# Performance work log

Hardware: AMD Instinct MI355X
Metric: run time of the kernel (lower is better)

The kernel has to match this reference:

```python
import jax, jax.numpy as jnp
import numpy as np

NUM_HEADS = 16
NHID = 64
D = NUM_HEADS * NHID  # 1024, also keys/query/values dim and out_dim
SL, BS = 2048, 32


def setup_inputs() -> dict:
    key = jax.random.key(0)
    ks = jax.random.split(key, 7)
    s = 1.0 / np.sqrt(D)
    return {
        "query": jax.random.normal(ks[0], (BS, D), jnp.float32),
        "keys": jax.random.normal(ks[1], (SL, BS, D), jnp.float32),
        "values": jax.random.normal(ks[2], (SL, BS, D), jnp.float32),
        "Wq": jax.random.normal(ks[3], (D, D), jnp.float32) * s,
        "Wk": jax.random.normal(ks[4], (D, D), jnp.float32) * s,
        "Wv": jax.random.normal(ks[5], (D, D), jnp.float32) * s,
        "Wo": jax.random.normal(ks[6], (D, D), jnp.float32) * s,
    }


def reference(query, keys, values, Wq, Wk, Wv, Wo):
    sl, bs, _ = keys.shape
    qp = query @ Wq.T                       # [bs, H*nhid]
    kp = keys @ Wk.T                        # [sl, bs, H*nhid]
    vp = values @ Wv.T                      # [sl, bs, H*nhid]
    # elementwise multiplicative score, reduced per head
    dot = (qp * kp).reshape(sl, bs, NUM_HEADS, NHID).sum(-1) / np.sqrt(NHID)
    # NOTE: original uses log_softmax (not softmax) over the sequence dim
    w = jax.nn.log_softmax(dot, axis=0)[..., None]        # [sl, bs, H, 1]
    attn = (w * vp.reshape(sl, bs, NUM_HEADS, NHID)).sum(0)  # [bs, H, nhid]
    return attn.reshape(bs, -1) @ Wo.T                     # [bs, D]
```

## Files before the change

### kernel.cpp

```cpp
#include <hip/hip_runtime.h>

#define SL  2048
#define BSZ 32
#define DIM 1024
#define NH  16
#define HD  64

typedef __attribute__((ext_vector_type(4))) float f32x4;
typedef __attribute__((ext_vector_type(8))) short s16x8;

static __device__ __forceinline__ short f2bf(float f) {
    union { float f; unsigned u; } v; v.f = f;
    unsigned r = (v.u + 0x7fffu + ((v.u >> 16) & 1u)) >> 16;
    return (short)r;
}

__global__ __launch_bounds__(256) void k_qu(const float* __restrict__ query,
                                            const float* __restrict__ Wq,
                                            const float* __restrict__ Wk,
                                            short* __restrict__ u) {
    int b = blockIdx.x & 31;
    int h = blockIdx.x >> 5;
    int t = threadIdx.x;
    __shared__ float red[256];
    __shared__ float sq[HD];
    {
        int i  = t >> 2;
        int kq = t & 3;
        const float* q = query + (size_t)b * DIM + kq * 256;
        const float* w = Wq + (size_t)(h * HD + i) * DIM + kq * 256;
        f32x4 acc = {0.f, 0.f, 0.f, 0.f};
#pragma unroll 4
        for (int k = 0; k < 256; k += 4)
            acc += *(const f32x4*)(q + k) * *(const f32x4*)(w + k);
        red[t] = acc[0] + acc[1] + acc[2] + acc[3];
    }
    __syncthreads();
    if (t < HD) sq[t] = (red[t*4] + red[t*4+1] + red[t*4+2] + red[t*4+3]) * 0.125f;
    __syncthreads();
    f32x4 acc = {0.f, 0.f, 0.f, 0.f};
    const float* wk = Wk + (size_t)(h * HD) * DIM;
#pragma unroll 8
    for (int i = 0; i < HD; ++i) {
        float s = sq[i];
        const float* row = wk + (size_t)i * DIM;
        acc[0] += s * row[t];
        acc[1] += s * row[t + 256];
        acc[2] += s * row[t + 512];
        acc[3] += s * row[t + 768];
    }
    short* ub = u + ((size_t)(b * NH + h)) * DIM;
    ub[t]       = f2bf(acc[0]);
    ub[t + 256] = f2bf(acc[1]);
    ub[t + 512] = f2bf(acc[2]);
    ub[t + 768] = f2bf(acc[3]);
}

__global__ __launch_bounds__(256, 4) void k_dot(const float* __restrict__ keys,
                                                const short* __restrict__ u,
                                                float* __restrict__ dot,
                                                float2* __restrict__ part) {
    int b  = blockIdx.x & 31;
    int st = blockIdx.x >> 5;
    int s0 = st * 64;
    __shared__ short ulds[NH][DIM + 8];
    {
        const uint4* src = (const uint4*)(u + (size_t)b * NH * DIM);
        for (int idx = threadIdx.x; idx < NH * DIM / 8; idx += 256) {
            int row = idx >> 7;
            int col = (idx & 127) * 8;
            *(uint4*)&ulds[row][col] = src[idx];
        }
    }
    __syncthreads();
    int lane = threadIdx.x & 63;
    int wave = threadIdx.x >> 6;
    int lrow = lane & 15;
    int kgrp = lane >> 4;
    f32x4 acc = {0.f, 0.f, 0.f, 0.f};
    const float* ka = keys + ((size_t)(s0 + wave * 16 + lrow) * BSZ + b) * DIM;
#pragma unroll 4
    for (int k0 = 0; k0 < DIM; k0 += 32) {
        int kj = k0 + kgrp * 8;
        s16x8 bf = *(const s16x8*)&ulds[lrow][kj];
        f32x4 a0 = *(const f32x4*)(ka + kj);
        f32x4 a1 = *(const f32x4*)(ka + kj + 4);
        s16x8 af;
        af[0]=f2bf(a0[0]); af[1]=f2bf(a0[1]); af[2]=f2bf(a0[2]); af[3]=f2bf(a0[3]);
        af[4]=f2bf(a1[0]); af[5]=f2bf(a1[1]); af[6]=f2bf(a1[2]); af[7]=f2bf(a1[3]);
        acc = __builtin_amdgcn_mfma_f32_16x16x32_bf16(af, bf, acc, 0, 0, 0);
    }
    size_t obase = ((size_t)b * SL + (s0 + wave * 16 + kgrp * 4)) * NH + lrow;
#pragma unroll
    for (int r = 0; r < 4; ++r)
        dot[obase + (size_t)r * NH] = acc[r];

    __shared__ float mred[4][16], lred[4][16];
    float m = fmaxf(fmaxf(acc[0], acc[1]), fmaxf(acc[2], acc[3]));
    m = fmaxf(m, __shfl_xor(m, 16));
    m = fmaxf(m, __shfl_xor(m, 32));
    if (lane < 16) mred[wave][lrow] = m;
    __syncthreads();
    float mb = fmaxf(fmaxf(mred[0][lrow], mred[1][lrow]),
                     fmaxf(mred[2][lrow], mred[3][lrow]));
    float l = __expf(acc[0]-mb) + __expf(acc[1]-mb) + __expf(acc[2]-mb) + __expf(acc[3]-mb);
    l += __shfl_xor(l, 16);
    l += __shfl_xor(l, 32);
    if (lane < 16) lred[wave][lrow] = l;
    __syncthreads();
    int t = threadIdx.x;
    if (t < 16) {
        float mbb = fmaxf(fmaxf(mred[0][t], mred[1][t]), fmaxf(mred[2][t], mred[3][t]));
        float lb  = lred[0][t] + lred[1][t] + lred[2][t] + lred[3][t];
        part[((size_t)b * 32 + st) * 16 + t] = make_float2(mbb, lb);
    }
}

__global__ __launch_bounds__(256, 4) void k_z(const float* __restrict__ values,
                                              const float* __restrict__ w,
                                              const float2* __restrict__ part,
                                              float* __restrict__ z) {
    int x  = blockIdx.x;
    int b  = x & 31;
    int jc = (x >> 5) & 15;
    int sh = x >> 9;
    int t  = threadIdx.x;
    int ssub = t >> 4;
    int jq = t & 15;
    int j = jc * 64 + jq * 4;
    int wv = __builtin_amdgcn_readfirstlane(t >> 6);
    int lane = t & 63;

    __shared__ float wlds[128 * 16];
    __shared__ float Tl[16];
    __shared__ float mred8[8][16], lred8[8][16];
    __shared__ f32x4 redW[4][16][16];
    __shared__ f32x4 redV[4][16];

    if (t < 128) {
        int h = t & 15, g = t >> 4;
        const float2* pb = part + (size_t)b * 32 * 16 + h;
        float2 p0 = pb[(g*4+0)*16], p1 = pb[(g*4+1)*16],
               p2 = pb[(g*4+2)*16], p3 = pb[(g*4+3)*16];
        float M = fmaxf(fmaxf(p0.x, p1.x), fmaxf(p2.x, p3.x));
        float L = p0.y*__expf(p0.x-M) + p1.y*__expf(p1.x-M)
                + p2.y*__expf(p2.x-M) + p3.y*__expf(p3.x-M);
        mred8[g][h] = M; lred8[g][h] = L;
    }
    __syncthreads();
    if (t < 16) {
        float M = mred8[0][t];
#pragma unroll
        for (int g = 1; g < 8; ++g) M = fmaxf(M, mred8[g][t]);
        float L = 0.f;
#pragma unroll
        for (int g = 0; g < 8; ++g) L += lred8[g][t] * __expf(mred8[g][t] - M);
        Tl[t] = M + __logf(L);
    }

    f32x4 acc[NH];
#pragma unroll
    for (int h = 0; h < NH; ++h) acc[h] = (f32x4){0.f,0.f,0.f,0.f};
    f32x4 accV = {0.f,0.f,0.f,0.f};

    const float* vbase = values + (size_t)b * DIM + j;
    const float* wbase = w + ((size_t)b * SL + sh * 1024) * NH;

    for (int ph = 0; ph < 8; ++ph) {
        __syncthreads();
        {
            const f32x4* src = (const f32x4*)(wbase + ph * 128 * NH);
            f32x4* dst = (f32x4*)wlds;
            dst[t]       = src[t];
            dst[t + 256] = src[t + 256];
        }
        __syncthreads();
        int sbase = sh * 1024 + ph * 128;
#pragma unroll 4
        for (int it = 0; it < 8; ++it) {
            int s_loc = it * 16 + ssub;
            f32x4 v = *(const f32x4*)(vbase + (size_t)(sbase + s_loc) * (BSZ * DIM));
            const float* wr = wlds + s_loc * 16;
#pragma unroll
            for (int h = 0; h < NH; ++h) {
                float wh = wr[h];
                acc[h] += v * wh;
            }
            accV += v;
        }
    }

#pragma unroll
    for (int h = 0; h < NH; ++h) {
#pragma unroll
        for (int e = 0; e < 4; ++e) {
            float x0 = acc[h][e];
            x0 += __shfl_xor(x0, 16);
            x0 += __shfl_xor(x0, 32);
            acc[h][e] = x0;
        }
    }
#pragma unroll
    for (int e = 0; e < 4; ++e) {
        float x0 = accV[e];
        x0 += __shfl_xor(x0, 16);
        x0 += __shfl_xor(x0, 32);
        accV[e] = x0;
    }
    if (lane < 16) {
#pragma unroll
        for (int h = 0; h < NH; ++h) redW[wv][h][lane] = acc[h];
        redV[wv][lane] = accV;
    }
    __syncthreads();
    int h2 = t >> 4, q = t & 15;
    f32x4 sumW = redW[0][h2][q] + redW[1][h2][q] + redW[2][h2][q] + redW[3][h2][q];
    f32x4 sumV = redV[0][q] + redV[1][q] + redV[2][q] + redV[3][q];
    float Th = Tl[h2];
    f32x4 zv = sumW - Th * sumV;
    float* zp = z + (size_t)sh * (BSZ * NH * DIM);
    *(f32x4*)(zp + ((size_t)(b * NH + h2)) * DIM + jc * 64 + q * 4) = zv;
}

template<bool DUAL>
__global__ __launch_bounds__(256) void k_gemm(const float* __restrict__ A,
                                              const float* __restrict__ A2,
                                              const float* __restrict__ W,
                                              float* __restrict__ O,
                                              int rmul, int hsel) {
    int oc = blockIdx.x & 15;
    int b  = blockIdx.x >> 4;
    int wv = __builtin_amdgcn_readfirstlane(threadIdx.x >> 6);
    int lane = threadIdx.x & 63;
    int o = oc * 64 + lane;
    int row = b * rmul + (hsel ? oc : 0);
    const float* arow  = A + (size_t)row * DIM + wv * 256;
    const float* a2row = DUAL ? (A2 + (size_t)row * DIM + wv * 256) : nullptr;
    const float* wrow  = W + (size_t)o * DIM + wv * 256;
    f32x4 acc = {0.f, 0.f, 0.f, 0.f};
#pragma unroll 4
    for (int k = 0; k < 256; k += 4) {
        f32x4 a = *(const f32x4*)(arow + k);
        if (DUAL) a += *(const f32x4*)(a2row + k);
        f32x4 w = *(const f32x4*)(wrow + k);
        acc += a * w;
    }
    __shared__ float red[4][64];
    red[wv][lane] = acc[0] + acc[1] + acc[2] + acc[3];
    __syncthreads();
    int t = threadIdx.x;
    if (t < 64)
        O[(size_t)b * DIM + oc * 64 + t] = red[0][t] + red[1][t] + red[2][t] + red[3][t];
}

extern "C" void kernel_launch(void* const* d_in, const int* in_sizes, int n_in,
                              void* d_out, int out_size, void* d_ws, size_t ws_size,
                              hipStream_t stream) {
    const float* query  = (const float*)d_in[0];
    const float* keys   = (const float*)d_in[1];
    const float* values = (const float*)d_in[2];
    const float* Wq = (const float*)d_in[3];
    const float* Wk = (const float*)d_in[4];
    const float* Wv = (const float*)d_in[5];
    const float* Wo = (const float*)d_in[6];
    float* out = (float*)d_out;

    char* ws = (char*)d_ws;
    short*  u    = (short*)(ws + 0);
    float*  dotb = (float*)(ws + (1 << 20));
    float*  z0   = (float*)(ws + (5 << 20));
    float*  z1   = (float*)(ws + (7 << 20));
    float*  attn = (float*)(ws + (9 << 20));
    float2* part = (float2*)(ws + (9 << 20) + (128 << 10));

    hipLaunchKernelGGL(k_qu,          dim3(512),  dim3(256), 0, stream, query, Wq, Wk, u);
    hipLaunchKernelGGL(k_dot,         dim3(1024), dim3(256), 0, stream, keys, u, dotb, part);
    hipLaunchKernelGGL(k_z,           dim3(1024), dim3(256), 0, stream, values, dotb, part, z0);
    hipLaunchKernelGGL(k_gemm<true>,  dim3(512),  dim3(256), 0, stream, z0, z1, Wv, attn, 16, 1);
    hipLaunchKernelGGL(k_gemm<false>, dim3(512),  dim3(256), 0, stream, attn, nullptr, Wo, out, 1, 0);
}
```

Measured before the change: 207.9 us.

## Restructure dot, value-reduction and Wv projection kernels with new work split

The dot kernel now processes 16 sequence rows per block (4096 blocks). Each block stages bf16-converted keys in LDS, and the four waves split the K dimension and reduce their MFMA partials through shared memory. The value-weighted reduction becomes k_zpart: 256 blocks of 512 threads, each streaming 256 sequence steps with float2 loads, writing 8 sequence-split partials plus value sums. The log-sum-exp finalisation and the partial combine move into the Wv GEMM kernel, which removes the separate normalisation from the z kernel. This trades more workspace traffic (8 partial z buffers) and low block count in k_zpart for better occupancy in the dot stage.

```diff
diff --git a/kernel.cpp b/kernel.cpp
--- a/kernel.cpp
+++ b/kernel.cpp
@@ -56,197 +56,199 @@
     ub[t + 768] = f2bf(acc[3]);
 }
 
-__global__ __launch_bounds__(256, 4) void k_dot(const float* __restrict__ keys,
-                                                const short* __restrict__ u,
-                                                float* __restrict__ dot,
-                                                float2* __restrict__ part) {
+__global__ __launch_bounds__(256) void k_dot2(const float* __restrict__ keys,
+                                              const short* __restrict__ u,
+                                              float* __restrict__ dot,
+                                              float2* __restrict__ part) {
     int b  = blockIdx.x & 31;
     int st = blockIdx.x >> 5;
-    int s0 = st * 64;
+    int s0 = st * 16;
     __shared__ short ulds[NH][DIM + 8];
+    __shared__ short klds[16][DIM + 8];
+    __shared__ f32x4 redc[4][64];
+    int t = threadIdx.x;
+    int w = t >> 6, l = t & 63;
+
     {
         const uint4* src = (const uint4*)(u + (size_t)b * NH * DIM);
-        for (int idx = threadIdx.x; idx < NH * DIM / 8; idx += 256) {
+        for (int idx = t; idx < NH * DIM / 8; idx += 256) {
             int row = idx >> 7;
             int col = (idx & 127) * 8;
             *(uint4*)&ulds[row][col] = src[idx];
         }
     }
-    __syncthreads();
-    int lane = threadIdx.x & 63;
-    int wave = threadIdx.x >> 6;
-    int lrow = lane & 15;
-    int kgrp = lane >> 4;
+#pragma unroll
+    for (int r = 0; r < 4; ++r) {
+        int srow = w * 4 + r;
+        const float* kr = keys + ((size_t)(s0 + srow) * BSZ + b) * DIM;
+#pragma unroll
+        for (int kq = 0; kq < 4; ++kq) {
+            f32x4 v = *(const f32x4*)(kr + kq * 256 + l * 4);
+            ushort4 o;
+            o.x = (unsigned short)f2bf(v[0]);
+            o.y = (unsigned short)f2bf(v[1]);
+            o.z = (unsigned short)f2bf(v[2]);
+            o.w = (unsigned short)f2bf(v[3]);
+            *(ushort4*)&klds[srow][kq * 256 + l * 4] = o;
+        }
+    }
+    __syncthreads();
+
+    int lrow = l & 15, kgrp = l >> 4;
     f32x4 acc = {0.f, 0.f, 0.f, 0.f};
-    const float* ka = keys + ((size_t)(s0 + wave * 16 + lrow) * BSZ + b) * DIM;
+#pragma unroll
+    for (int kk = 0; kk < 8; ++kk) {
+        int kj = w * 256 + kk * 32 + kgrp * 8;
+        s16x8 af = *(const s16x8*)&klds[lrow][kj];
+        s16x8 bf = *(const s16x8*)&ulds[lrow][kj];
+        acc = __builtin_amdgcn_mfma_f32_16x16x32_bf16(af, bf, acc, 0, 0, 0);
+    }
+    redc[w][l] = acc;
+    __syncthreads();
+    if (t < 64) {
+        f32x4 sum = redc[0][t] + redc[1][t] + redc[2][t] + redc[3][t];
+        int lr = t & 15, kg = t >> 4;
+        size_t obase = ((size_t)b * SL + (s0 + kg * 4)) * NH + lr;
+#pragma unroll
+        for (int r = 0; r < 4; ++r)
+            dot[obase + (size_t)r * NH] = sum[r];
+        float m = fmaxf(fmaxf(sum[0], sum[1]), fmaxf(sum[2], sum[3]));
+        m = fmaxf(m, __shfl_xor(m, 16));
+        m = fmaxf(m, __shfl_xor(m, 32));
+        float lsum = __expf(sum[0]-m) + __expf(sum[1]-m) + __expf(sum[2]-m) + __expf(sum[3]-m);
+        lsum += __shfl_xor(lsum, 16);
+        lsum += __shfl_xor(lsum, 32);
+        if (t < 16)
+            part[((size_t)b * 128 + st) * 16 + t] = make_float2(m, lsum);
+    }
+}
+
+__global__ __launch_bounds__(512) void k_zpart(const float* __restrict__ values,
+                                               const float* __restrict__ dotb,
+                                               float* __restrict__ zpart,
+                                               float* __restrict__ svpart) {
+    int b  = blockIdx.x & 31;
+    int sq = blockIdx.x >> 5;
+    int t  = threadIdx.x;
+    __shared__ f32x4 wlds4[1024];
+    {
+        const f32x4* src = (const f32x4*)(dotb + ((size_t)b * SL + sq * 256) * NH);
+        wlds4[t]       = src[t];
+        wlds4[t + 512] = src[t + 512];
+    }
+    __syncthreads();
+    const float* wlds = (const float*)wlds4;
+
+    float ax[NH], ay[NH];
+#pragma unroll
+    for (int h = 0; h < NH; ++h) { ax[h] = 0.f; ay[h] = 0.f; }
+    float svx = 0.f, svy = 0.f;
+
+    const float* vbase = values + ((size_t)(sq * 256) * BSZ + b) * DIM + t * 2;
+#pragma unroll 8
+    for (int s = 0; s < 256; ++s) {
+        float2 v = *(const float2*)(vbase + (size_t)s * (BSZ * DIM));
+        const float* wr = wlds + s * 16;
+#pragma unroll
+        for (int h = 0; h < NH; ++h) {
+            float wh = wr[h];
+            ax[h] += v.x * wh;
+            ay[h] += v.y * wh;
+        }
+        svx += v.x;
+        svy += v.y;
+    }
+    float* zp = zpart + (size_t)(sq * 32 + b) * NH * DIM + t * 2;
+#pragma unroll
+    for (int h = 0; h < NH; ++h) {
+        float2 o; o.x = ax[h]; o.y = ay[h];
+        *(float2*)(zp + (size_t)h * DIM) = o;
+    }
+    float2 sv; sv.x = svx; sv.y = svy;
+    *(float2*)(svpart + (size_t)(sq * 32 + b) * DIM + t * 2) = sv;
+}
+
+__global__ __launch_bounds__(256) void k_attn(const float* __restrict__ zpart,
+                                              const float* __restrict__ svpart,
+                                              const float2* __restrict__ part,
+                                              const float* __restrict__ Wv,
+                                              float* __restrict__ attn) {
+    int oc = blockIdx.x & 15;
+    int b  = blockIdx.x >> 4;
+    int t  = threadIdx.x;
+    int wv = t >> 6, l = t & 63;
+    __shared__ float mred[16][16], lred[16][16];
+    __shared__ float Tl[16];
+    __shared__ float arow[DIM];
+    __shared__ float red[4][64];
+    {
+        int h = t & 15, g = t >> 4;
+        const float2* pb = part + (size_t)b * 128 * 16 + h;
+        float M = -1e30f;
+        float2 ps[8];
+#pragma unroll
+        for (int i = 0; i < 8; ++i) ps[i] = pb[(size_t)(g * 8 + i) * 16];
+#pragma unroll
+        for (int i = 0; i < 8; ++i) M = fmaxf(M, ps[i].x);
+        float L = 0.f;
+#pragma unroll
+        for (int i = 0; i < 8; ++i) L += ps[i].y * __expf(ps[i].x - M);
+        mred[g][h] = M; lred[g][h] = L;
+    }
+    __syncthreads();
+    if (t < 16) {
+        float M = mred[0][t];
+#pragma unroll
+        for (int g = 1; g < 16; ++g) M = fmaxf(M, mred[g][t]);
+        float L = 0.f;
+#pragma unroll
+        for (int g = 0; g < 16; ++g) L += lred[g][t] * __expf(mred[g][t] - M);
+        Tl[t] = M + __logf(L);
+    }
+    __syncthreads();
+    {
+        int k = wv * 256 + l * 4;
+        f32x4 a = {0.f,0.f,0.f,0.f}, sv = {0.f,0.f,0.f,0.f};
+#pragma unroll
+        for (int p = 0; p < 8; ++p) {
+            a  += *(const f32x4*)(zpart + ((size_t)((p * 32 + b) * NH + oc)) * DIM + k);
+            sv += *(const f32x4*)(svpart + (size_t)(p * 32 + b) * DIM + k);
+        }
+        a -= Tl[oc] * sv;
+        *(f32x4*)&arow[k] = a;
+    }
+    __syncthreads();
+    const float* wr = Wv + (size_t)(oc * 64 + l) * DIM + wv * 256;
+    const float* ar = arow + wv * 256;
+    f32x4 acc = {0.f,0.f,0.f,0.f};
 #pragma unroll 4
-    for (int k0 = 0; k0 < DIM; k0 += 32) {
-        int kj = k0 + kgrp * 8;
-        s16x8 bf = *(const s16x8*)&ulds[lrow][kj];
-        f32x4 a0 = *(const f32x4*)(ka + kj);
-        f32x4 a1 = *(const f32x4*)(ka + kj + 4);
-        s16x8 af;
-        af[0]=f2bf(a0[0]); af[1]=f2bf(a0[1]); af[2]=f2bf(a0[2]); af[3]=f2bf(a0[3]);
-        af[4]=f2bf(a1[0]); af[5]=f2bf(a1[1]); af[6]=f2bf(a1[2]); af[7]=f2bf(a1[3]);
-        acc = __builtin_amdgcn_mfma_f32_16x16x32_bf16(af, bf, acc, 0, 0, 0);
-    }
-    size_t obase = ((size_t)b * SL + (s0 + wave * 16 + kgrp * 4)) * NH + lrow;
-#pragma unroll
-    for (int r = 0; r < 4; ++r)
-        dot[obase + (size_t)r * NH] = acc[r];
-
-    __shared__ float mred[4][16], lred[4][16];
-    float m = fmaxf(fmaxf(acc[0], acc[1]), fmaxf(acc[2], acc[3]));
-    m = fmaxf(m, __shfl_xor(m, 16));
-    m = fmaxf(m, __shfl_xor(m, 32));
-    if (lane < 16) mred[wave][lrow] = m;
-    __syncthreads();
-    float mb = fmaxf(fmaxf(mred[0][lrow], mred[1][lrow]),
-                     fmaxf(mred[2][lrow], mred[3][lrow]));
-    float l = __expf(acc[0]-mb) + __expf(acc[1]-mb) + __expf(acc[2]-mb) + __expf(acc[3]-mb);
-    l += __shfl_xor(l, 16);
-    l += __shfl_xor(l, 32);
-    if (lane < 16) lred[wave][lrow] = l;
-    __syncthreads();
-    int t = threadIdx.x;
-    if (t < 16) {
-        float mbb = fmaxf(fmaxf(mred[0][t], mred[1][t]), fmaxf(mred[2][t], mred[3][t]));
-        float lb  = lred[0][t] + lred[1][t] + lred[2][t] + lred[3][t];
-        part[((size_t)b * 32 + st) * 16 + t] = make_float2(mbb, lb);
-    }
-}
-
-__global__ __launch_bounds__(256, 4) void k_z(const float* __restrict__ values,
-                                              const float* __restrict__ w,
-                                              const float2* __restrict__ part,
-                                              float* __restrict__ z) {
-    int x  = blockIdx.x;
-    int b  = x & 31;
-    int jc = (x >> 5) & 15;
-    int sh = x >> 9;
-    int t  = threadIdx.x;
-    int ssub = t >> 4;
-    int jq = t & 15;
-    int j = jc * 64 + jq * 4;
-    int wv = __builtin_amdgcn_readfirstlane(t >> 6);
-    int lane = t & 63;
-
-    __shared__ float wlds[128 * 16];
-    __shared__ float Tl[16];
-    __shared__ float mred8[8][16], lred8[8][16];
-    __shared__ f32x4 redW[4][16][16];
-    __shared__ f32x4 redV[4][16];
-
-    if (t < 128) {
-        int h = t & 15, g = t >> 4;
-        const float2* pb = part + (size_t)b * 32 * 16 + h;
-        float2 p0 = pb[(g*4+0)*16], p1 = pb[(g*4+1)*16],
-               p2 = pb[(g*4+2)*16], p3 = pb[(g*4+3)*16];
-        float M = fmaxf(fmaxf(p0.x, p1.x), fmaxf(p2.x, p3.x));
-        float L = p0.y*__expf(p0.x-M) + p1.y*__expf(p1.x-M)
-                + p2.y*__expf(p2.x-M) + p3.y*__expf(p3.x-M);
-        mred8[g][h] = M; lred8[g][h] = L;
-    }
-    __syncthreads();
-    if (t < 16) {
-        float M = mred8[0][t];
-#pragma unroll
-        for (int g = 1; g < 8; ++g) M = fmaxf(M, mred8[g][t]);
-        float L = 0.f;
-#pragma unroll
-        for (int g = 0; g < 8; ++g) L += lred8[g][t] * __expf(mred8[g][t] - M);
-        Tl[t] = M + __logf(L);
-    }
-
-    f32x4 acc[NH];
-#pragma unroll
-    for (int h = 0; h < NH; ++h) acc[h] = (f32x4){0.f,0.f,0.f,0.f};
-    f32x4 accV = {0.f,0.f,0.f,0.f};
-
-    const float* vbase = values + (size_t)b * DIM + j;
-    const float* wbase = w + ((size_t)b * SL + sh * 1024) * NH;
-
-    for (int ph = 0; ph < 8; ++ph) {
-        __syncthreads();
-        {
-            const f32x4* src = (const f32x4*)(wbase + ph * 128 * NH);
-            f32x4* dst = (f32x4*)wlds;
-            dst[t]       = src[t];
-            dst[t + 256] = src[t + 256];
-        }
-        __syncthreads();
-        int sbase = sh * 1024 + ph * 128;
-#pragma unroll 4
-        for (int it = 0; it < 8; ++it) {
-            int s_loc = it * 16 + ssub;
-            f32x4 v = *(const f32x4*)(vbase + (size_t)(sbase + s_loc) * (BSZ * DIM));
-            const float* wr = wlds + s_loc * 16;
-#pragma unroll
-            for (int h = 0; h < NH; ++h) {
-                float wh = wr[h];
-                acc[h] += v * wh;
-            }
-            accV += v;
-        }
-    }
-
-#pragma unroll
-    for (int h = 0; h < NH; ++h) {
-#pragma unroll
-        for (int e = 0; e < 4; ++e) {
-            float x0 = acc[h][e];
-            x0 += __shfl_xor(x0, 16);
-            x0 += __shfl_xor(x0, 32);
-            acc[h][e] = x0;
-        }
-    }
-#pragma unroll
-    for (int e = 0; e < 4; ++e) {
-        float x0 = accV[e];
-        x0 += __shfl_xor(x0, 16);
-        x0 += __shfl_xor(x0, 32);
-        accV[e] = x0;
-    }
-    if (lane < 16) {
-#pragma unroll
-        for (int h = 0; h < NH; ++h) redW[wv][h][lane] = acc[h];
-        redV[wv][lane] = accV;
-    }
-    __syncthreads();
-    int h2 = t >> 4, q = t & 15;
-    f32x4 sumW = redW[0][h2][q] + redW[1][h2][q] + redW[2][h2][q] + redW[3][h2][q];
-    f32x4 sumV = redV[0][q] + redV[1][q] + redV[2][q] + redV[3][q];
-    float Th = Tl[h2];
-    f32x4 zv = sumW - Th * sumV;
-    float* zp = z + (size_t)sh * (BSZ * NH * DIM);
-    *(f32x4*)(zp + ((size_t)(b * NH + h2)) * DIM + jc * 64 + q * 4) = zv;
-}
-
-template<bool DUAL>
-__global__ __launch_bounds__(256) void k_gemm(const float* __restrict__ A,
-                                              const float* __restrict__ A2,
-                                              const float* __restrict__ W,
-                                              float* __restrict__ O,
-                                              int rmul, int hsel) {
+    for (int kk = 0; kk < 256; kk += 4)
+        acc += *(const f32x4*)(ar + kk) * *(const f32x4*)(wr + kk);
+    red[wv][l] = acc[0] + acc[1] + acc[2] + acc[3];
+    __syncthreads();
+    if (t < 64)
+        attn[(size_t)b * DIM + oc * 64 + t] = red[0][t] + red[1][t] + red[2][t] + red[3][t];
+}
+
+__global__ __launch_bounds__(256) void k_out(const float* __restrict__ A,
+                                             const float* __restrict__ W,
+                                             float* __restrict__ O) {
     int oc = blockIdx.x & 15;
     int b  = blockIdx.x >> 4;
     int wv = __builtin_amdgcn_readfirstlane(threadIdx.x >> 6);
-    int lane = threadIdx.x & 63;
-    int o = oc * 64 + lane;
-    int row = b * rmul + (hsel ? oc : 0);
-    const float* arow  = A + (size_t)row * DIM + wv * 256;
-    const float* a2row = DUAL ? (A2 + (size_t)row * DIM + wv * 256) : nullptr;
-    const float* wrow  = W + (size_t)o * DIM + wv * 256;
+    int l  = threadIdx.x & 63;
+    int o  = oc * 64 + l;
+    const float* arow = A + (size_t)b * DIM + wv * 256;
+    const float* wrow = W + (size_t)o * DIM + wv * 256;
     f32x4 acc = {0.f, 0.f, 0.f, 0.f};
 #pragma unroll 4
     for (int k = 0; k < 256; k += 4) {
         f32x4 a = *(const f32x4*)(arow + k);
-        if (DUAL) a += *(const f32x4*)(a2row + k);
         f32x4 w = *(const f32x4*)(wrow + k);
         acc += a * w;
     }
     __shared__ float red[4][64];
-    red[wv][lane] = acc[0] + acc[1] + acc[2] + acc[3];
+    red[wv][l] = acc[0] + acc[1] + acc[2] + acc[3];
     __syncthreads();
     int t = threadIdx.x;
     if (t < 64)
@@ -266,16 +268,16 @@
     float* out = (float*)d_out;
 
     char* ws = (char*)d_ws;
-    short*  u    = (short*)(ws + 0);
-    float*  dotb = (float*)(ws + (1 << 20));
-    float*  z0   = (float*)(ws + (5 << 20));
-    float*  z1   = (float*)(ws + (7 << 20));
-    float*  attn = (float*)(ws + (9 << 20));
-    float2* part = (float2*)(ws + (9 << 20) + (128 << 10));
-
-    hipLaunchKernelGGL(k_qu,          dim3(512),  dim3(256), 0, stream, query, Wq, Wk, u);
-    hipLaunchKernelGGL(k_dot,         dim3(1024), dim3(256), 0, stream, keys, u, dotb, part);
-    hipLaunchKernelGGL(k_z,           dim3(1024), dim3(256), 0, stream, values, dotb, part, z0);
-    hipLaunchKernelGGL(k_gemm<true>,  dim3(512),  dim3(256), 0, stream, z0, z1, Wv, attn, 16, 1);
-    hipLaunchKernelGGL(k_gemm<false>, dim3(512),  dim3(256), 0, stream, attn, nullptr, Wo, out, 1, 0);
-}
+    short*  u      = (short*)(ws + 0);
+    float*  dotb   = (float*)(ws + (1 << 20));
+    float2* part   = (float2*)(ws + (5 << 20));
+    float*  zpart  = (float*)(ws + (5 << 20) + (512 << 10));
+    float*  svpart = (float*)(ws + (21 << 20) + (512 << 10));
+    float*  attn   = (float*)(ws + (22 << 20) + (512 << 10));
+
+    hipLaunchKernelGGL(k_qu,    dim3(512),  dim3(256), 0, stream, query, Wq, Wk, u);
+    hipLaunchKernelGGL(k_dot2,  dim3(4096), dim3(256), 0, stream, keys, u, dotb, part);
+    hipLaunchKernelGGL(k_zpart, dim3(256),  dim3(512), 0, stream, values, dotb, zpart, svpart);
+    hipLaunchKernelGGL(k_attn,  dim3(512),  dim3(256), 0, stream, zpart, svpart, part, Wv, attn);
+    hipLaunchKernelGGL(k_out,   dim3(512),  dim3(256), 0, stream, attn, Wo, out);
+}
```

New measurement: 212.3 us. 2.1% more time.

## Fuse five kernels into one cooperative persistent kernel with grid syncs

Applied to the files above, without the earlier changes.

Merges the five phase kernels into a single cooperative launch that separates phases with grid.sync(), keeping a multi-kernel fallback if the cooperative launch fails. Shared memory is unioned across phases. The u tile in LDS now uses an XOR swizzle in place of row padding to avoid bank conflicts. This removes per-launch gaps and tail drain between kernels. In exchange, the LDS union raises the per-block footprint, so occupancy is limited to the largest phase, and grid-wide barriers carry their own cost.

```diff
diff --git a/kernel.cpp b/kernel.cpp
--- a/kernel.cpp
+++ b/kernel.cpp
@@ -1,4 +1,7 @@
 #include <hip/hip_runtime.h>
+#include <hip/hip_cooperative_groups.h>
+
+namespace cg = cooperative_groups;
 
 #define SL  2048
 #define BSZ 32
@@ -15,15 +18,25 @@
     return (short)r;
 }
 
-__global__ __launch_bounds__(256) void k_qu(const float* __restrict__ query,
-                                            const float* __restrict__ Wq,
-                                            const float* __restrict__ Wk,
-                                            short* __restrict__ u) {
-    int b = blockIdx.x & 31;
-    int h = blockIdx.x >> 5;
-    int t = threadIdx.x;
-    __shared__ float red[256];
-    __shared__ float sq[HD];
+union SharedU {
+    struct { float red[256]; float sq[HD]; } p1;
+    union {
+        short ulds[NH * 1024];
+        struct { float mred[4][16]; float lred[4][16]; } r;
+    } p2;
+    struct { float wlds[128 * 16]; float Tl[16];
+             float mred8[8][16]; float lred8[8][16];
+             f32x4 redW[4][16][16]; f32x4 redV[4][16]; } p3;
+    struct { float red[4][64]; } p45;
+};
+
+static __device__ __forceinline__ void phase_u(int blk, int t, SharedU* sh,
+                                               const float* __restrict__ query,
+                                               const float* __restrict__ Wq,
+                                               const float* __restrict__ Wk,
+                                               short* __restrict__ u) {
+    int b = blk & 31;
+    int h = blk >> 5;
     {
         int i  = t >> 2;
         int kq = t & 3;
@@ -33,16 +46,18 @@
 #pragma unroll 4
         for (int k = 0; k < 256; k += 4)
             acc += *(const f32x4*)(q + k) * *(const f32x4*)(w + k);
-        red[t] = acc[0] + acc[1] + acc[2] + acc[3];
-    }
-    __syncthreads();
-    if (t < HD) sq[t] = (red[t*4] + red[t*4+1] + red[t*4+2] + red[t*4+3]) * 0.125f;
+        sh->p1.red[t] = acc[0] + acc[1] + acc[2] + acc[3];
+    }
+    __syncthreads();
+    if (t < HD)
+        sh->p1.sq[t] = (sh->p1.red[t*4] + sh->p1.red[t*4+1] +
+                        sh->p1.red[t*4+2] + sh->p1.red[t*4+3]) * 0.125f;
     __syncthreads();
     f32x4 acc = {0.f, 0.f, 0.f, 0.f};
     const float* wk = Wk + (size_t)(h * HD) * DIM;
 #pragma unroll 8
     for (int i = 0; i < HD; ++i) {
-        float s = sq[i];
+        float s = sh->p1.sq[i];
         const float* row = wk + (size_t)i * DIM;
         acc[0] += s * row[t];
         acc[1] += s * row[t + 256];
@@ -56,33 +71,35 @@
     ub[t + 768] = f2bf(acc[3]);
 }
 
-__global__ __launch_bounds__(256, 4) void k_dot(const float* __restrict__ keys,
-                                                const short* __restrict__ u,
-                                                float* __restrict__ dot,
-                                                float2* __restrict__ part) {
-    int b  = blockIdx.x & 31;
-    int st = blockIdx.x >> 5;
+static __device__ __forceinline__ void phase_dot(int blk, int t, SharedU* sh,
+                                                 const float* __restrict__ keys,
+                                                 const short* __restrict__ u,
+                                                 float* __restrict__ dotb,
+                                                 float2* __restrict__ part) {
+    int b  = blk & 31;
+    int st = blk >> 5;
     int s0 = st * 64;
-    __shared__ short ulds[NH][DIM + 8];
+    short* ulds = sh->p2.ulds;
     {
         const uint4* src = (const uint4*)(u + (size_t)b * NH * DIM);
-        for (int idx = threadIdx.x; idx < NH * DIM / 8; idx += 256) {
+        for (int idx = t; idx < NH * DIM / 8; idx += 256) {
             int row = idx >> 7;
-            int col = (idx & 127) * 8;
-            *(uint4*)&ulds[row][col] = src[idx];
+            int c   = idx & 127;
+            *(uint4*)&ulds[row * 1024 + ((c ^ (row & 7)) << 3)] = src[idx];
         }
     }
     __syncthreads();
-    int lane = threadIdx.x & 63;
-    int wave = threadIdx.x >> 6;
+    int lane = t & 63;
+    int wave = t >> 6;
     int lrow = lane & 15;
     int kgrp = lane >> 4;
+    int swz  = (lrow & 7) << 3;
     f32x4 acc = {0.f, 0.f, 0.f, 0.f};
     const float* ka = keys + ((size_t)(s0 + wave * 16 + lrow) * BSZ + b) * DIM;
 #pragma unroll 4
     for (int k0 = 0; k0 < DIM; k0 += 32) {
         int kj = k0 + kgrp * 8;
-        s16x8 bf = *(const s16x8*)&ulds[lrow][kj];
+        s16x8 bf = *(const s16x8*)&ulds[lrow * 1024 + (kj ^ swz)];
         f32x4 a0 = *(const f32x4*)(ka + kj);
         f32x4 a1 = *(const f32x4*)(ka + kj + 4);
         s16x8 af;
@@ -93,69 +110,63 @@
     size_t obase = ((size_t)b * SL + (s0 + wave * 16 + kgrp * 4)) * NH + lrow;
 #pragma unroll
     for (int r = 0; r < 4; ++r)
-        dot[obase + (size_t)r * NH] = acc[r];
-
-    __shared__ float mred[4][16], lred[4][16];
+        dotb[obase + (size_t)r * NH] = acc[r];
+
+    __syncthreads();
     float m = fmaxf(fmaxf(acc[0], acc[1]), fmaxf(acc[2], acc[3]));
     m = fmaxf(m, __shfl_xor(m, 16));
     m = fmaxf(m, __shfl_xor(m, 32));
-    if (lane < 16) mred[wave][lrow] = m;
-    __syncthreads();
-    float mb = fmaxf(fmaxf(mred[0][lrow], mred[1][lrow]),
-                     fmaxf(mred[2][lrow], mred[3][lrow]));
-    float l = __expf(acc[0]-mb) + __expf(acc[1]-mb) + __expf(acc[2]-mb) + __expf(acc[3]-mb);
-    l += __shfl_xor(l, 16);
-    l += __shfl_xor(l, 32);
-    if (lane < 16) lred[wave][lrow] = l;
-    __syncthreads();
-    int t = threadIdx.x;
+    if (lane < 16) sh->p2.r.mred[wave][lrow] = m;
+    __syncthreads();
+    float mb = fmaxf(fmaxf(sh->p2.r.mred[0][lrow], sh->p2.r.mred[1][lrow]),
+                     fmaxf(sh->p2.r.mred[2][lrow], sh->p2.r.mred[3][lrow]));
+    float lsum = __expf(acc[0]-mb) + __expf(acc[1]-mb) + __expf(acc[2]-mb) + __expf(acc[3]-mb);
+    lsum += __shfl_xor(lsum, 16);
+    lsum += __shfl_xor(lsum, 32);
+    if (lane < 16) sh->p2.r.lred[wave][lrow] = lsum;
+    __syncthreads();
     if (t < 16) {
-        float mbb = fmaxf(fmaxf(mred[0][t], mred[1][t]), fmaxf(mred[2][t], mred[3][t]));
-        float lb  = lred[0][t] + lred[1][t] + lred[2][t] + lred[3][t];
+        float mbb = fmaxf(fmaxf(sh->p2.r.mred[0][t], sh->p2.r.mred[1][t]),
+                          fmaxf(sh->p2.r.mred[2][t], sh->p2.r.mred[3][t]));
+        float lb  = sh->p2.r.lred[0][t] + sh->p2.r.lred[1][t]
+                  + sh->p2.r.lred[2][t] + sh->p2.r.lred[3][t];
         part[((size_t)b * 32 + st) * 16 + t] = make_float2(mbb, lb);
     }
 }
 
-__global__ __launch_bounds__(256, 4) void k_z(const float* __restrict__ values,
-                                              const float* __restrict__ w,
-                                              const float2* __restrict__ part,
-                                              float* __restrict__ z) {
-    int x  = blockIdx.x;
-    int b  = x & 31;
-    int jc = (x >> 5) & 15;
-    int sh = x >> 9;
-    int t  = threadIdx.x;
+static __device__ __forceinline__ void phase_z(int blk, int t, SharedU* sh,
+                                               const float* __restrict__ values,
+                                               const float* __restrict__ dotb,
+                                               const float2* __restrict__ part,
+                                               float* __restrict__ z) {
+    int b   = blk & 31;
+    int jc  = (blk >> 5) & 15;
+    int shf = blk >> 9;
     int ssub = t >> 4;
     int jq = t & 15;
     int j = jc * 64 + jq * 4;
     int wv = __builtin_amdgcn_readfirstlane(t >> 6);
     int lane = t & 63;
 
-    __shared__ float wlds[128 * 16];
-    __shared__ float Tl[16];
-    __shared__ float mred8[8][16], lred8[8][16];
-    __shared__ f32x4 redW[4][16][16];
-    __shared__ f32x4 redV[4][16];
-
     if (t < 128) {
         int h = t & 15, g = t >> 4;
         const float2* pb = part + (size_t)b * 32 * 16 + h;
         float2 p0 = pb[(g*4+0)*16], p1 = pb[(g*4+1)*16],
-               p2 = pb[(g*4+2)*16], p3 = pb[(g*4+3)*16];
-        float M = fmaxf(fmaxf(p0.x, p1.x), fmaxf(p2.x, p3.x));
+               p2 = pb[(g*4+2)*16], p3v = pb[(g*4+3)*16];
+        float M = fmaxf(fmaxf(p0.x, p1.x), fmaxf(p2.x, p3v.x));
         float L = p0.y*__expf(p0.x-M) + p1.y*__expf(p1.x-M)
-                + p2.y*__expf(p2.x-M) + p3.y*__expf(p3.x-M);
-        mred8[g][h] = M; lred8[g][h] = L;
+                + p2.y*__expf(p2.x-M) + p3v.y*__expf(p3v.x-M);
+        sh->p3.mred8[g][h] = M; sh->p3.lred8[g][h] = L;
     }
     __syncthreads();
     if (t < 16) {
-        float M = mred8[0][t];
-#pragma unroll
-        for (int g = 1; g < 8; ++g) M = fmaxf(M, mred8[g][t]);
+        float M = sh->p3.mred8[0][t];
+#pragma unroll
+        for (int g = 1; g < 8; ++g) M = fmaxf(M, sh->p3.mred8[g][t]);
         float L = 0.f;
 #pragma unroll
-        for (int g = 0; g < 8; ++g) L += lred8[g][t] * __expf(mred8[g][t] - M);
-        Tl[t] = M + __logf(L);
+        for (int g = 0; g < 8; ++g) L += sh->p3.lred8[g][t] * __expf(sh->p3.mred8[g][t] - M);
+        sh->p3.Tl[t] = M + __logf(L);
     }
 
     f32x4 acc[NH];
@@ -164,23 +175,23 @@
     f32x4 accV = {0.f,0.f,0.f,0.f};
 
     const float* vbase = values + (size_t)b * DIM + j;
-    const float* wbase = w + ((size_t)b * SL + sh * 1024) * NH;
+    const float* wbase = dotb + ((size_t)b * SL + shf * 1024) * NH;
 
     for (int ph = 0; ph < 8; ++ph) {
         __syncthreads();
         {
             const f32x4* src = (const f32x4*)(wbase + ph * 128 * NH);
-            f32x4* dst = (f32x4*)wlds;
+            f32x4* dst = (f32x4*)sh->p3.wlds;
             dst[t]       = src[t];
             dst[t + 256] = src[t + 256];
         }
         __syncthreads();
-        int sbase = sh * 1024 + ph * 128;
+        int sbase = shf * 1024 + ph * 128;
 #pragma unroll 4
         for (int it = 0; it < 8; ++it) {
             int s_loc = it * 16 + ssub;
             f32x4 v = *(const f32x4*)(vbase + (size_t)(sbase + s_loc) * (BSZ * DIM));
-            const float* wr = wlds + s_loc * 16;
+            const float* wr = sh->p3.wlds + s_loc * 16;
 #pragma unroll
             for (int h = 0; h < NH; ++h) {
                 float wh = wr[h];
@@ -209,48 +220,118 @@
     }
     if (lane < 16) {
 #pragma unroll
-        for (int h = 0; h < NH; ++h) redW[wv][h][lane] = acc[h];
-        redV[wv][lane] = accV;
+        for (int h = 0; h < NH; ++h) sh->p3.redW[wv][h][lane] = acc[h];
+        sh->p3.redV[wv][lane] = accV;
     }
     __syncthreads();
     int h2 = t >> 4, q = t & 15;
-    f32x4 sumW = redW[0][h2][q] + redW[1][h2][q] + redW[2][h2][q] + redW[3][h2][q];
-    f32x4 sumV = redV[0][q] + redV[1][q] + redV[2][q] + redV[3][q];
-    float Th = Tl[h2];
+    f32x4 sumW = sh->p3.redW[0][h2][q] + sh->p3.redW[1][h2][q]
+               + sh->p3.redW[2][h2][q] + sh->p3.redW[3][h2][q];
+    f32x4 sumV = sh->p3.redV[0][q] + sh->p3.redV[1][q]
+               + sh->p3.redV[2][q] + sh->p3.redV[3][q];
+    float Th = sh->p3.Tl[h2];
     f32x4 zv = sumW - Th * sumV;
-    float* zp = z + (size_t)sh * (BSZ * NH * DIM);
+    float* zp = z + (size_t)shf * (BSZ * NH * DIM);
     *(f32x4*)(zp + ((size_t)(b * NH + h2)) * DIM + jc * 64 + q * 4) = zv;
 }
 
-template<bool DUAL>
-__global__ __launch_bounds__(256) void k_gemm(const float* __restrict__ A,
-                                              const float* __restrict__ A2,
-                                              const float* __restrict__ W,
-                                              float* __restrict__ O,
-                                              int rmul, int hsel) {
-    int oc = blockIdx.x & 15;
-    int b  = blockIdx.x >> 4;
-    int wv = __builtin_amdgcn_readfirstlane(threadIdx.x >> 6);
-    int lane = threadIdx.x & 63;
+static __device__ __forceinline__ void phase_attn(int blk, int t, SharedU* sh,
+                                                  const float* __restrict__ z,
+                                                  const float* __restrict__ Wv,
+                                                  float* __restrict__ attn) {
+    int oc = blk & 15;
+    int b  = blk >> 4;
+    int wv = __builtin_amdgcn_readfirstlane(t >> 6);
+    int lane = t & 63;
     int o = oc * 64 + lane;
-    int row = b * rmul + (hsel ? oc : 0);
-    const float* arow  = A + (size_t)row * DIM + wv * 256;
-    const float* a2row = DUAL ? (A2 + (size_t)row * DIM + wv * 256) : nullptr;
-    const float* wrow  = W + (size_t)o * DIM + wv * 256;
+    int row = b * 16 + oc;
+    const float* arow  = z + (size_t)row * DIM + wv * 256;
+    const float* a2row = z + (size_t)(BSZ * NH * DIM) + (size_t)row * DIM + wv * 256;
+    const float* wrow  = Wv + (size_t)o * DIM + wv * 256;
     f32x4 acc = {0.f, 0.f, 0.f, 0.f};
 #pragma unroll 4
     for (int k = 0; k < 256; k += 4) {
-        f32x4 a = *(const f32x4*)(arow + k);
-        if (DUAL) a += *(const f32x4*)(a2row + k);
-        f32x4 w = *(const f32x4*)(wrow + k);
-        acc += a * w;
-    }
-    __shared__ float red[4][64];
-    red[wv][lane] = acc[0] + acc[1] + acc[2] + acc[3];
-    __syncthreads();
+        f32x4 a = *(const f32x4*)(arow + k) + *(const f32x4*)(a2row + k);
+        acc += a * *(const f32x4*)(wrow + k);
+    }
+    sh->p45.red[wv][lane] = acc[0] + acc[1] + acc[2] + acc[3];
+    __syncthreads();
+    if (t < 64)
+        attn[(size_t)b * DIM + oc * 64 + t] =
+            sh->p45.red[0][t] + sh->p45.red[1][t] + sh->p45.red[2][t] + sh->p45.red[3][t];
+}
+
+static __device__ __forceinline__ void phase_out(int blk, int t, SharedU* sh,
+                                                 const float* __restrict__ attn,
+                                                 const float* __restrict__ Wo,
+                                                 float* __restrict__ out) {
+    int oc = blk & 15;
+    int b  = blk >> 4;
+    int wv = __builtin_amdgcn_readfirstlane(t >> 6);
+    int lane = t & 63;
+    int o = oc * 64 + lane;
+    const float* arow = attn + (size_t)b * DIM + wv * 256;
+    const float* wrow = Wo + (size_t)o * DIM + wv * 256;
+    f32x4 acc = {0.f, 0.f, 0.f, 0.f};
+#pragma unroll 4
+    for (int k = 0; k < 256; k += 4)
+        acc += *(const f32x4*)(arow + k) * *(const f32x4*)(wrow + k);
+    sh->p45.red[wv][lane] = acc[0] + acc[1] + acc[2] + acc[3];
+    __syncthreads();
+    if (t < 64)
+        out[(size_t)b * DIM + oc * 64 + t] =
+            sh->p45.red[0][t] + sh->p45.red[1][t] + sh->p45.red[2][t] + sh->p45.red[3][t];
+}
+
+__global__ __launch_bounds__(256, 4) void k_mega(
+    const float* __restrict__ query, const float* __restrict__ keys,
+    const float* __restrict__ values, const float* __restrict__ Wq,
+    const float* __restrict__ Wk, const float* __restrict__ Wv,
+    const float* __restrict__ Wo, short* __restrict__ u,
+    float* __restrict__ dotb, float2* __restrict__ part,
+    float* __restrict__ z, float* __restrict__ attn,
+    float* __restrict__ out)
+{
+    cg::grid_group grid = cg::this_grid();
+    __shared__ SharedU sh;
+    int blk = blockIdx.x;
     int t = threadIdx.x;
-    if (t < 64)
-        O[(size_t)b * DIM + oc * 64 + t] = red[0][t] + red[1][t] + red[2][t] + red[3][t];
+
+    if (blk < 512) phase_u(blk, t, &sh, query, Wq, Wk, u);
+    grid.sync();
+    phase_dot(blk, t, &sh, keys, u, dotb, part);
+    grid.sync();
+    phase_z(blk, t, &sh, values, dotb, part, z);
+    grid.sync();
+    if (blk < 512) phase_attn(blk, t, &sh, z, Wv, attn);
+    grid.sync();
+    if (blk < 512) phase_out(blk, t, &sh, attn, Wo, out);
+}
+
+__global__ __launch_bounds__(256, 4) void k_p1(const float* query, const float* Wq,
+                                               const float* Wk, short* u) {
+    __shared__ SharedU sh;
+    phase_u(blockIdx.x, threadIdx.x, &sh, query, Wq, Wk, u);
+}
+__global__ __launch_bounds__(256, 4) void k_p2(const float* keys, const short* u,
+                                               float* dotb, float2* part) {
+    __shared__ SharedU sh;
+    phase_dot(blockIdx.x, threadIdx.x, &sh, keys, u, dotb, part);
+}
+__global__ __launch_bounds__(256, 4) void k_p3(const float* values, const float* dotb,
+                                               const float2* part, float* z) {
+    __shared__ SharedU sh;
+    phase_z(blockIdx.x, threadIdx.x, &sh, values, dotb, part, z);
+}
+__global__ __launch_bounds__(256, 4) void k_p4(const float* z, const float* Wv,
+                                               float* attn) {
+    __shared__ SharedU sh;
+    phase_attn(blockIdx.x, threadIdx.x, &sh, z, Wv, attn);
+}
+__global__ __launch_bounds__(256, 4) void k_p5(const float* attn, const float* Wo,
+                                               float* out) {
+    __shared__ SharedU sh;
+    phase_out(blockIdx.x, threadIdx.x, &sh, attn, Wo, out);
 }
 
 extern "C" void kernel_launch(void* const* d_in, const int* in_sizes, int n_in,
@@ -263,19 +344,27 @@
     const float* Wk = (const float*)d_in[4];
     const float* Wv = (const float*)d_in[5];
     const float* Wo = (const float*)d_in[6];
-    float* out = (float*)d_out;
+    float* outp = (float*)d_out;
 
     char* ws = (char*)d_ws;
     short*  u    = (short*)(ws + 0);
     float*  dotb = (float*)(ws + (1 << 20));
-    float*  z0   = (float*)(ws + (5 << 20));
-    float*  z1   = (float*)(ws + (7 << 20));
-    float*  attn = (float*)(ws + (9 << 20));
-    float2* part = (float2*)(ws + (9 << 20) + (128 << 10));
-
-    hipLaunchKernelGGL(k_qu,          dim3(512),  dim3(256), 0, stream, query, Wq, Wk, u);
-    hipLaunchKernelGGL(k_dot,         dim3(1024), dim3(256), 0, stream, keys, u, dotb, part);
-    hipLaunchKernelGGL(k_z,           dim3(1024), dim3(256), 0, stream, values, dotb, part, z0);
-    hipLaunchKernelGGL(k_gemm<true>,  dim3(512),  dim3(256), 0, stream, z0, z1, Wv, attn, 16, 1);
-    hipLaunchKernelGGL(k_gemm<false>, dim3(512),  dim3(256), 0, stream, attn, nullptr, Wo, out, 1, 0);
-}
+    float2* part = (float2*)(ws + (5 << 20));
+    float*  z    = (float*)(ws + (5 << 20) + (512 << 10));
+    float*  attn = (float*)(ws + (9 << 20) + (512 << 10));
+
+    void* args[13] = {
+        (void*)&query, (void*)&keys, (void*)&values,
+        (void*)&Wq, (void*)&Wk, (void*)&Wv, (void*)&Wo,
+        (void*)&u, (void*)&dotb, (void*)&part, (void*)&z, (void*)&attn, (void*)&outp
+    };
+    hipError_t err = hipLaunchCooperativeKernel((const void*)k_mega, dim3(1024),
+                                                dim3(256), args, 0, stream);
+    if (err != hipSuccess) {
+        hipLaunchKernelGGL(k_p1, dim3(512),  dim3(256), 0, stream, query, Wq, Wk, u);
+        hipLaunchKernelGGL(k_p2, dim3(1024), dim3(256), 0, stream, keys, u, dotb, part);
+        hipLaunchKernelGGL(k_p3, dim3(1024), dim3(256), 0, stream, values, dotb, part, z);
+        hipLaunchKernelGGL(k_p4, dim3(512),  dim3(256), 0, stream, z, Wv, attn);
+        hipLaunchKernelGGL(k_p5, dim3(512),  dim3(256), 0, stream, attn, Wo, outp);
+    }
+}
```

Measured after the change: 703.4 us. 3.38x slower.
